# Kernel tuning notes

Measured on AMD Instinct MI355X. Metric: run time of the kernel, lower is better.

Reference implementation:

```python
import jax, jax.numpy as jnp
import numpy as np
import math

D_MODEL = 2048
NUM_HEADS = 16
D_HEAD = D_MODEL // NUM_HEADS
MAX_SEQ_LEN = 2048
THETA = 10000.0
B, T = 2, 2048


def setup_inputs() -> dict:
    key = jax.random.key(0)
    ks = jax.random.split(key, 5)
    s = 1.0 / math.sqrt(D_MODEL)
    return {
        "x": jax.random.normal(ks[0], (B, T, D_MODEL), dtype=jnp.float32),
        "token_positions": jnp.arange(T, dtype=jnp.int64 if jax.config.jax_enable_x64 else jnp.int32),
        "Wq": jax.random.normal(ks[1], (D_MODEL, D_MODEL), dtype=jnp.float32) * s,
        "Wk": jax.random.normal(ks[2], (D_MODEL, D_MODEL), dtype=jnp.float32) * s,
        "Wv": jax.random.normal(ks[3], (D_MODEL, D_MODEL), dtype=jnp.float32) * s,
        "Wproj": jax.random.normal(ks[4], (D_MODEL, D_MODEL), dtype=jnp.float32) * s,
    }


def _rope_tables(dtype):
    inv_freq = 1.0 / (THETA ** (jnp.arange(0, D_HEAD, 2, dtype=jnp.float32) / D_HEAD))
    angle = jnp.arange(MAX_SEQ_LEN, dtype=jnp.float32)[:, None] * inv_freq[None, :]  # [S, d/2]
    return jnp.cos(angle).astype(dtype), jnp.sin(angle).astype(dtype)


def _apply_rope(x, cos, sin):
    # x: [B, H, T, d_head]; cos/sin: [T, d_head/2] (broadcast over B,H)
    x1 = x[..., 0::2]
    x2 = x[..., 1::2]
    o1 = x1 * cos - x2 * sin
    o2 = x1 * sin + x2 * cos
    return jnp.stack([o1, o2], axis=-1).reshape(x.shape)


def reference(x, token_positions, Wq, Wk, Wv, Wproj):
    Bx, Tx, D = x.shape
    # Linear layers: weight [out, in], no bias
    q = (x @ Wq.T).reshape(Bx, Tx, NUM_HEADS, D_HEAD).transpose(0, 2, 1, 3)
    k = (x @ Wk.T).reshape(Bx, Tx, NUM_HEADS, D_HEAD).transpose(0, 2, 1, 3)
    v = (x @ Wv.T).reshape(Bx, Tx, NUM_HEADS, D_HEAD).transpose(0, 2, 1, 3)

    cos_t, sin_t = _rope_tables(x.dtype)
    cos = cos_t[token_positions]  # [T, d_head/2]
    sin = sin_t[token_positions]
    q = _apply_rope(q, cos, sin)
    k = _apply_rope(k, cos, sin)

    scale = 1.0 / math.sqrt(D_HEAD)
    scores = jnp.einsum("bhqd,bhkd->bhqk", q, k) * scale
    causal = jnp.tril(jnp.ones((Tx, Tx), dtype=bool))
    scores = jnp.where(causal, scores, -jnp.inf)
    attn = jax.nn.softmax(scores, axis=-1)
    o = jnp.einsum("bhqk,bhkd->bhqd", attn, v)  # [B, H, T, d_head]
    o = o.transpose(0, 2, 1, 3).reshape(Bx, Tx, D)
    return o @ Wproj.T
```

## Files before the change

### kernel.cpp

```cpp
#include <hip/hip_runtime.h>
#include <hip/hip_bf16.h>

#define DM    2048
#define NH    16
#define DHD   128
#define TSEQ  2048
#define NBB   2
#define NTOK  (NBB*TSEQ)

typedef __attribute__((ext_vector_type(8))) short bf16x8;
typedef __attribute__((ext_vector_type(4))) float f32x4;

typedef __attribute__((address_space(1))) const void GVoid;
typedef __attribute__((address_space(3))) void LVoid;
#define GLOAD16(SRC, DST) __builtin_amdgcn_global_load_lds((GVoid*)(SRC), (LVoid*)(DST), 16, 0, 0)

__device__ __forceinline__ unsigned short f2bf(float f) {
  union { float f; unsigned u; } v; v.f = f;
  unsigned r = v.u + 0x7fffu + ((v.u >> 16) & 1u);
  return (unsigned short)(r >> 16);
}
__device__ __forceinline__ float bf2f(unsigned short h) {
  union { unsigned u; float f; } v; v.u = ((unsigned)h) << 16;
  return v.f;
}

#define QSCALE (0.08838834764831845f * 1.4426950408889634f)

__global__ void cvt_kernel(const float* __restrict__ in, unsigned short* __restrict__ out, int n4) {
  int i = blockIdx.x * blockDim.x + threadIdx.x;
  int stride = gridDim.x * blockDim.x;
  for (; i < n4; i += stride) {
    float4 v = reinterpret_cast<const float4*>(in)[i];
    ushort4 o;
    o.x = f2bf(v.x); o.y = f2bf(v.y); o.z = f2bf(v.z); o.w = f2bf(v.w);
    reinterpret_cast<ushort4*>(out)[i] = o;
  }
}

__global__ void cvt4_kernel(const float* __restrict__ a, const float* __restrict__ b,
                           const float* __restrict__ c, const float* __restrict__ d,
                           unsigned short* __restrict__ out, int n4per) {
  const float* in = (blockIdx.y == 0) ? a : (blockIdx.y == 1) ? b : (blockIdx.y == 2) ? c : d;
  unsigned short* o = out + (size_t)blockIdx.y * (size_t)n4per * 4;
  int i = blockIdx.x * blockDim.x + threadIdx.x;
  int stride = gridDim.x * blockDim.x;
  for (; i < n4per; i += stride) {
    float4 v = reinterpret_cast<const float4*>(in)[i];
    ushort4 ov;
    ov.x = f2bf(v.x); ov.y = f2bf(v.y); ov.z = f2bf(v.z); ov.w = f2bf(v.w);
    reinterpret_cast<ushort4*>(o)[i] = ov;
  }
}

__global__ void rope_table_kernel(const int* __restrict__ pos, float* __restrict__ ctab, float* __restrict__ stab) {
  int idx = blockIdx.x * blockDim.x + threadIdx.x;
  if (idx >= TSEQ * 64) return;
  int i = idx & 63;
  int t = idx >> 6;
  float freq = expf(-(2.0f * i / 128.0f) * 9.210340371976184f);
  float ang = (float)pos[t] * freq;
  ctab[idx] = cosf(ang);
  stab[idx] = sinf(ang);
}

__global__ void vtrans_kernel(const unsigned short* __restrict__ Vb, unsigned short* __restrict__ VTt) {
  __shared__ unsigned short tile[32][33];
  int t0 = blockIdx.x * 32, d0 = blockIdx.y * 32, bh = blockIdx.z;
  int h = bh & (NH - 1), b = bh >> 4;
  int tx = threadIdx.x, ty = threadIdx.y;
  #pragma unroll
  for (int i = 0; i < 4; i++) {
    int tt = t0 + ty + i * 8;
    tile[ty + i * 8][tx] = Vb[(size_t)(b * TSEQ + tt) * DM + h * DHD + d0 + tx];
  }
  __syncthreads();
  #pragma unroll
  for (int i = 0; i < 4; i++) {
    int d = d0 + ty + i * 8;
    VTt[((size_t)bh * DHD + d) * TSEQ + t0 + tx] = tile[tx][ty + i * 8];
  }
}

#define GBM 128
#define GBN 256
#define GBK 32
#define LDSB ((GBM + GBN) * GBK)
template<int MODE>
__global__ __launch_bounds__(512, 4) void gemmk(
    const unsigned short* __restrict__ A,
    const unsigned short* __restrict__ Bt,
    void* __restrict__ Cp,
    unsigned short* __restrict__ QrO, unsigned short* __restrict__ KrO,
    const float* __restrict__ ct, const float* __restrict__ st,
    int K, int N, int NBN) {
  __shared__ unsigned short lds[3 * LDSB];
  const int t = threadIdx.x;
  const int lane = t & 63, w = t >> 6;
  const int wr = w >> 2, wc = w & 3;
  const int lr = lane & 15, lg = lane >> 4;
  const int nwg = gridDim.x;
  const int swz = (blockIdx.x & 7) * (nwg >> 3) + (blockIdx.x >> 3);
  const int m0 = (swz / NBN) * GBM;
  const int n0g = (swz % NBN) * GBN;
  const int NT = K / GBK;

  f32x4 acc[4][4] = {};

  auto stage = [&](int kt, int b) {
    unsigned short* dst = &lds[b * LDSB];
    const size_t k0 = (size_t)kt * GBK;
    {
      int row = t >> 2, slot = t & 3;
      int ss = slot ^ ((row >> 1) & 3);
      GLOAD16(A + (size_t)(m0 + row) * K + k0 + ss * 8, dst + (size_t)(w * 64) * 8);
    }
    unsigned short* dstB = dst + GBM * GBK;
    #pragma unroll
    for (int c = 0; c < 2; c++) {
      int ci = c * 512 + t;
      int row = ci >> 2, slot = ci & 3;
      int ss = slot ^ ((row >> 1) & 3);
      GLOAD16(Bt + (size_t)(n0g + row) * K + k0 + ss * 8, dstB + (size_t)(c * 512 + w * 64) * 8);
    }
  };

  const unsigned short* buf = nullptr;
  auto ldA = [&](int mi) -> bf16x8 {
    int r = wr * 64 + mi * 16 + lr;
    int cb = (lg * 16) ^ (((r >> 1) & 3) << 4);
    return *(const bf16x8*)((const char*)buf + r * 64 + cb);
  };
  auto ldB = [&](int ni) -> bf16x8 {
    int r = wc * 64 + ni * 16 + lr;
    int cb = (lg * 16) ^ (((r >> 1) & 3) << 4);
    return *(const bf16x8*)((const char*)(buf + GBM * GBK) + r * 64 + cb);
  };

  stage(0, 0);
  stage(1, 1);

  for (int kt = 0; kt < NT; kt++) {
    if (kt + 1 < NT) { asm volatile("s_waitcnt vmcnt(3)" ::: "memory"); }
    else             { asm volatile("s_waitcnt vmcnt(0)" ::: "memory"); }
    __builtin_amdgcn_s_barrier();
    buf = &lds[(kt % 3) * LDSB];

    bf16x8 bfr[4], afr[4];
    #pragma unroll
    for (int ni = 0; ni < 4; ni++) bfr[ni] = ldB(ni);
    #pragma unroll
    for (int mi = 0; mi < 4; mi++) afr[mi] = ldA(mi);
    if (kt + 2 < NT) stage(kt + 2, (kt + 2) % 3);
    asm volatile("s_waitcnt lgkmcnt(0)" ::: "memory");
    __builtin_amdgcn_sched_barrier(0);
    __builtin_amdgcn_s_setprio(1);
    #pragma unroll
    for (int mi = 0; mi < 4; mi++)
      #pragma unroll
      for (int ni = 0; ni < 4; ni++)
        acc[mi][ni] = __builtin_amdgcn_mfma_f32_16x16x32_bf16(afr[mi], bfr[ni], acc[mi][ni], 0, 0, 0);
    __builtin_amdgcn_s_setprio(0);
  }

  if (MODE == 0) {
    #pragma unroll
    for (int mi = 0; mi < 4; mi++)
      #pragma unroll
      for (int j = 0; j < 4; j++) {
        int row = m0 + wr * 64 + mi * 16 + lg * 4 + j;
        #pragma unroll
        for (int ni = 0; ni < 4; ni++) {
          int cg = n0g + wc * 64 + ni * 16 + lr;
          ((float*)Cp)[(size_t)row * N + cg] = acc[mi][ni][j];
        }
      }
  } else {
    const int sel = n0g >> 11;
    if (sel == 2) {
      #pragma unroll
      for (int mi = 0; mi < 4; mi++)
        #pragma unroll
        for (int j = 0; j < 4; j++) {
          int row = m0 + wr * 64 + mi * 16 + lg * 4 + j;
          #pragma unroll
          for (int ni = 0; ni < 4; ni++) {
            int c2 = (n0g + wc * 64 + ni * 16 + lr) & 2047;
            ((unsigned short*)Cp)[(size_t)row * DM + c2] = f2bf(acc[mi][ni][j]);
          }
        }
    } else {
      unsigned short* dst = sel ? KrO : QrO;
      const float qm = sel ? 1.0f : QSCALE;
      #pragma unroll
      for (int mi = 0; mi < 4; mi++)
        #pragma unroll
        for (int j = 0; j < 4; j++) {
          int row = m0 + wr * 64 + mi * 16 + lg * 4 + j;
          int bb = row >> 11, tt = row & (TSEQ - 1);
          #pragma unroll
          for (int ni = 0; ni < 4; ni++) {
            int c2 = (n0g + wc * 64 + ni * 16 + lr) & 2047;
            int d = c2 & 127, hh = c2 >> 7;
            float v = acc[mi][ni][j];
            float px = __shfl_xor(v, 1);
            float cc = ct[tt * 64 + (d >> 1)], ss = st[tt * 64 + (d >> 1)];
            float o = (d & 1) ? (px * ss + v * cc) : (v * cc - px * ss);
            dst[(((size_t)(bb * NH + hh)) * TSEQ + tt) * DHD + d] = f2bf(o * qm);
          }
        }
    }
  }
}

__global__ __launch_bounds__(512, 4) void attn_kernel(
    const unsigned short* __restrict__ Qr,
    const unsigned short* __restrict__ Kr,
    const unsigned short* __restrict__ VTt,
    unsigned short* __restrict__ Oa) {
  __shared__ unsigned short Ks[64 * 128];
  __shared__ unsigned short Vs[128 * 64];
  __shared__ unsigned short Ps[8 * 16 * 64];
  const int t = threadIdx.x;
  const int lane = t & 63, w = t >> 6;
  const int wv = w & 3, half = w >> 2;
  const int lr = lane & 15, lg = lane >> 4;
  const int p = blockIdx.x, bh = blockIdx.y;
  const int qA = p, qB = 31 - p;
  const int myq = half ? qA : qB;
  const int q0 = myq * 64;
  const int nt = myq + 1;
  const int ntB = qB + 1;
  const unsigned short* Qh = Qr + (size_t)bh * TSEQ * DHD;
  const unsigned short* Kh = Kr + (size_t)bh * TSEQ * DHD;
  const unsigned short* Vh = VTt + (size_t)bh * DHD * TSEQ;

  bf16x8 qf[4];
  #pragma unroll
  for (int ks = 0; ks < 4; ks++)
    qf[ks] = *(const bf16x8*)&Qh[((size_t)(q0 + wv * 16 + lr)) * DHD + ks * 32 + lg * 8];

  f32x4 oacc[8] = {};
  float ps[4] = {};
  unsigned short* Pw = &Ps[w * 16 * 64];

  for (int jt = 0; jt < ntB; jt++) {
    const int j0 = jt * 64;
    #pragma unroll
    for (int c = 0; c < 2; c++) {
      int ci = c * 512 + t;
      int row = ci >> 4, slot = ci & 15;
      GLOAD16(Kh + (size_t)(j0 + row) * DHD + (slot ^ (row & 7)) * 8,
              &Ks[(c * 512 + w * 64) * 8]);
    }
    #pragma unroll
    for (int c = 0; c < 2; c++) {
      int ci = c * 512 + t;
      int row = ci >> 3, slot = ci & 7;
      GLOAD16(Vh + (size_t)row * TSEQ + j0 + (slot ^ (row & 7)) * 8,
              &Vs[(c * 512 + w * 64) * 8]);
    }
    __syncthreads();
    if (jt < nt) {
      const bool diag = (jt == nt - 1);
      f32x4 sv[4] = {};
      #pragma unroll
      for (int n = 0; n < 4; n++) {
        #pragma unroll
        for (int ks = 0; ks < 4; ks++) {
          int row = n * 16 + lr;
          int byteoff = row * 256 + (((ks * 64 + lg * 16)) ^ ((row & 7) << 4));
          bf16x8 kf = *(const bf16x8*)((const char*)Ks + byteoff);
          sv[n] = __builtin_amdgcn_mfma_f32_16x16x32_bf16(qf[ks], kf, sv[n], 0, 0, 0);
        }
      }
      if (diag) {
        #pragma unroll
        for (int n = 0; n < 4; n++) {
          int kcol = j0 + n * 16 + lr;
          #pragma unroll
          for (int j = 0; j < 4; j++)
            if (kcol > q0 + wv * 16 + lg * 4 + j) sv[n][j] = -INFINITY;
        }
      }
      #pragma unroll
      for (int n = 0; n < 4; n++) {
        #pragma unroll
        for (int j = 0; j < 4; j++) {
          float pv = exp2f(sv[n][j]);
          ps[j] += pv;
          int prow = lg * 4 + j;
          int pcol = n * 16 + lr;
          int byteoff = (prow * 128 + pcol * 2) ^ ((prow & 7) << 4);
          *(unsigned short*)((char*)Pw + byteoff) = f2bf(pv);
        }
      }
      bf16x8 pa[2];
      #pragma unroll
      for (int kk = 0; kk < 2; kk++) {
        int byteoff = lr * 128 + (((kk * 64 + lg * 16)) ^ ((lr & 7) << 4));
        pa[kk] = *(const bf16x8*)((const char*)Pw + byteoff);
      }
      #pragma unroll
      for (int n2 = 0; n2 < 8; n2++) {
        #pragma unroll
        for (int kk = 0; kk < 2; kk++) {
          int row = n2 * 16 + lr;
          int byteoff = row * 128 + (((kk * 64 + lg * 16)) ^ ((row & 7) << 4));
          bf16x8 vf = *(const bf16x8*)((const char*)Vs + byteoff);
          oacc[n2] = __builtin_amdgcn_mfma_f32_16x16x32_bf16(pa[kk], vf, oacc[n2], 0, 0, 0);
        }
      }
    }
    __syncthreads();
  }

  #pragma unroll
  for (int m = 1; m < 16; m <<= 1)
    #pragma unroll
    for (int j = 0; j < 4; j++) ps[j] += __shfl_xor(ps[j], m);
  const int h = bh & (NH - 1), b = bh >> 4;
  #pragma unroll
  for (int j = 0; j < 4; j++) {
    float inv = 1.0f / ps[j];
    int tt = q0 + wv * 16 + lg * 4 + j;
    size_t base = ((size_t)(b * TSEQ + tt)) * DM + h * DHD;
    #pragma unroll
    for (int n2 = 0; n2 < 8; n2++)
      Oa[base + n2 * 16 + lr] = f2bf(oacc[n2][j] * inv);
  }
}

extern "C" void kernel_launch(void* const* d_in, const int* in_sizes, int n_in,
                              void* d_out, int out_size, void* d_ws, size_t ws_size,
                              hipStream_t stream) {
  const float* x  = (const float*)d_in[0];
  const int*   pos = (const int*)d_in[1];
  const float* Wq = (const float*)d_in[2];
  const float* Wk = (const float*)d_in[3];
  const float* Wv = (const float*)d_in[4];
  const float* Wp = (const float*)d_in[5];
  float* out = (float*)d_out;

  char* wsp = (char*)d_ws;
  auto alloc = [&](size_t bytes) { char* p = wsp; wsp += (bytes + 255) & ~(size_t)255; return p; };
  unsigned short* xb  = (unsigned short*)alloc((size_t)NTOK * DM * 2);
  unsigned short* wqb = (unsigned short*)alloc((size_t)DM * DM * 2);
  unsigned short* wkb = (unsigned short*)alloc((size_t)DM * DM * 2);
  unsigned short* wvb = (unsigned short*)alloc((size_t)DM * DM * 2);
  unsigned short* wpb = (unsigned short*)alloc((size_t)DM * DM * 2);
  unsigned short* Qb  = (unsigned short*)alloc((size_t)NTOK * DM * 2);
  unsigned short* Kb  = (unsigned short*)alloc((size_t)NTOK * DM * 2);
  unsigned short* Vb  = (unsigned short*)alloc((size_t)NTOK * DM * 2);
  unsigned short* VTt = (unsigned short*)alloc((size_t)NTOK * DM * 2);
  float* ctab = (float*)alloc((size_t)TSEQ * 64 * 4);
  float* stab = (float*)alloc((size_t)TSEQ * 64 * 4);
  unsigned short* Oa = xb;
  (void)wkb; (void)wvb;

  int n4x = NTOK * DM / 4, n4w = DM * DM / 4;
  cvt_kernel<<<2048, 256, 0, stream>>>(x, xb, n4x);
  cvt4_kernel<<<dim3(256, 4), 256, 0, stream>>>(Wq, Wk, Wv, Wp, wqb, n4w);
  rope_table_kernel<<<(TSEQ * 64) / 256, 256, 0, stream>>>(pos, ctab, stab);

  gemmk<1><<<(NTOK / GBM) * (3 * DM / GBN), 512, 0, stream>>>(
      xb, wqb, Vb, Qb, Kb, ctab, stab, DM, DM, 3 * DM / GBN);

  vtrans_kernel<<<dim3(TSEQ / 32, DHD / 32, NBB * NH), dim3(32, 8), 0, stream>>>(Vb, VTt);

  attn_kernel<<<dim3(16, NBB * NH), 512, 0, stream>>>(Qb, Kb, VTt, Oa);

  gemmk<0><<<(NTOK / GBM) * (DM / GBN), 512, 0, stream>>>(
      Oa, wpb, out, nullptr, nullptr, nullptr, nullptr, DM, DM, DM / GBN);
}
```

Baseline: 260.3 us.

## Split attention KV range across half-blocks and add 256x128 output GEMM

Attention now launches one block per (query tile, head) in descending-work order instead of pairing two query tiles per block. The two halves of the block each process half of the causal KV tiles using double LDS buffers, and their partial outputs and row sums are merged through LDS at the end. This is meant to improve load balance and parallelism. The output projection switches to a new 256x128-tile GEMM with a triple-buffered global-to-LDS pipeline and priority-raised MFMA phases. The costs are more blocks, an extra LDS reduction step, and higher LDS use.

```diff
diff --git a/kernel.cpp b/kernel.cpp
--- a/kernel.cpp
+++ b/kernel.cpp
@@ -213,24 +213,150 @@
   }
 }
 
+#define G2M 256
+#define G2N 128
+#define G2K 64
+__global__ __launch_bounds__(512, 2) void gemm256(
+    const unsigned short* __restrict__ A,
+    const unsigned short* __restrict__ Bt,
+    float* __restrict__ Cp, int K, int N, int NBN) {
+  __shared__ unsigned short lds[3 * (G2M + G2N) * G2K];
+  const int t = threadIdx.x;
+  const int lane = t & 63, w = t >> 6;
+  const int wr = w >> 2, wc = w & 3;
+  const int lr = lane & 15, lg = lane >> 4;
+  const int nwg = gridDim.x;
+  const int swz = (blockIdx.x & 7) * (nwg >> 3) + (blockIdx.x >> 3);
+  const int m0 = (swz / NBN) * G2M;
+  const int n0g = (swz % NBN) * G2N;
+  const int NT = K / G2K;
+
+  f32x4 acc[8][2] = {};
+
+  auto stageA = [&](int kt, int b) {
+    unsigned short* dst = &lds[b * (G2M + G2N) * G2K];
+    const size_t k0 = (size_t)kt * G2K;
+    #pragma unroll
+    for (int c = 0; c < 4; c++) {
+      int i = c * 512 + t;
+      int row = i >> 3, slot = i & 7;
+      int sslot = slot ^ (row & 7);
+      GLOAD16(A + (size_t)(m0 + row) * K + k0 + sslot * 8,
+              dst + (size_t)(c * 512 + w * 64) * 8);
+    }
+  };
+  auto stageB = [&](int kt, int b) {
+    unsigned short* dst = &lds[b * (G2M + G2N) * G2K + G2M * G2K];
+    const size_t k0 = (size_t)kt * G2K;
+    #pragma unroll
+    for (int c = 0; c < 2; c++) {
+      int i = c * 512 + t;
+      int row = i >> 3, slot = i & 7;
+      int sslot = slot ^ (row & 7);
+      GLOAD16(Bt + (size_t)(n0g + row) * K + k0 + sslot * 8,
+              dst + (size_t)(c * 512 + w * 64) * 8);
+    }
+  };
+
+  const unsigned short* bufA = nullptr;
+  const unsigned short* bufB = nullptr;
+  auto ldA = [&](int mi, int ks) -> bf16x8 {
+    int r = wr * 128 + mi * 16 + lr;
+    int cb = (ks * 64 + lg * 16) ^ ((r & 7) << 4);
+    return *(const bf16x8*)((const char*)bufA + r * 128 + cb);
+  };
+  auto ldB = [&](int ni, int ks) -> bf16x8 {
+    int r = wc * 32 + ni * 16 + lr;
+    int cb = (ks * 64 + lg * 16) ^ ((r & 7) << 4);
+    return *(const bf16x8*)((const char*)bufB + r * 128 + cb);
+  };
+
+  stageA(0, 0); stageB(0, 0);
+  stageA(1, 1); stageB(1, 1);
+
+  for (int kt = 0; kt < NT; kt++) {
+    if (kt + 1 < NT) { asm volatile("s_waitcnt vmcnt(6)" ::: "memory"); }
+    else             { asm volatile("s_waitcnt vmcnt(0)" ::: "memory"); }
+    __builtin_amdgcn_s_barrier();
+    const int b = kt % 3;
+    bufA = &lds[b * (G2M + G2N) * G2K];
+    bufB = bufA + G2M * G2K;
+    const int kt2 = kt + 2, b2 = kt2 % 3;
+
+    bf16x8 bfr[2][2], afr[4][2];
+    #pragma unroll
+    for (int ni = 0; ni < 2; ni++)
+      #pragma unroll
+      for (int ks = 0; ks < 2; ks++) bfr[ni][ks] = ldB(ni, ks);
+    #pragma unroll
+    for (int mi = 0; mi < 4; mi++)
+      #pragma unroll
+      for (int ks = 0; ks < 2; ks++) afr[mi][ks] = ldA(mi, ks);
+    if (kt2 < NT) stageA(kt2, b2);
+    asm volatile("s_waitcnt lgkmcnt(0)" ::: "memory");
+    __builtin_amdgcn_sched_barrier(0);
+    __builtin_amdgcn_s_setprio(1);
+    #pragma unroll
+    for (int mi = 0; mi < 4; mi++)
+      #pragma unroll
+      for (int ni = 0; ni < 2; ni++)
+        #pragma unroll
+        for (int ks = 0; ks < 2; ks++)
+          acc[mi][ni] = __builtin_amdgcn_mfma_f32_16x16x32_bf16(afr[mi][ks], bfr[ni][ks], acc[mi][ni], 0, 0, 0);
+    __builtin_amdgcn_s_setprio(0);
+    __builtin_amdgcn_s_barrier();
+
+    bf16x8 afr2[4][2];
+    #pragma unroll
+    for (int mi = 0; mi < 4; mi++)
+      #pragma unroll
+      for (int ks = 0; ks < 2; ks++) afr2[mi][ks] = ldA(mi + 4, ks);
+    if (kt2 < NT) stageB(kt2, b2);
+    asm volatile("s_waitcnt lgkmcnt(0)" ::: "memory");
+    __builtin_amdgcn_sched_barrier(0);
+    __builtin_amdgcn_s_setprio(1);
+    #pragma unroll
+    for (int mi = 0; mi < 4; mi++)
+      #pragma unroll
+      for (int ni = 0; ni < 2; ni++)
+        #pragma unroll
+        for (int ks = 0; ks < 2; ks++)
+          acc[mi + 4][ni] = __builtin_amdgcn_mfma_f32_16x16x32_bf16(afr2[mi][ks], bfr[ni][ks], acc[mi + 4][ni], 0, 0, 0);
+    __builtin_amdgcn_s_setprio(0);
+  }
+
+  #pragma unroll
+  for (int mi = 0; mi < 8; mi++)
+    #pragma unroll
+    for (int j = 0; j < 4; j++) {
+      int row = m0 + wr * 128 + mi * 16 + lg * 4 + j;
+      #pragma unroll
+      for (int ni = 0; ni < 2; ni++) {
+        int cg = n0g + wc * 32 + ni * 16 + lr;
+        Cp[(size_t)row * N + cg] = acc[mi][ni][j];
+      }
+    }
+}
+
 __global__ __launch_bounds__(512, 4) void attn_kernel(
     const unsigned short* __restrict__ Qr,
     const unsigned short* __restrict__ Kr,
     const unsigned short* __restrict__ VTt,
     unsigned short* __restrict__ Oa) {
-  __shared__ unsigned short Ks[64 * 128];
-  __shared__ unsigned short Vs[128 * 64];
+  __shared__ unsigned short Ks[2][64 * 128];
+  __shared__ unsigned short Vs[2][128 * 64];
   __shared__ unsigned short Ps[8 * 16 * 64];
   const int t = threadIdx.x;
   const int lane = t & 63, w = t >> 6;
   const int wv = w & 3, half = w >> 2;
+  const int th = t & 255;
   const int lr = lane & 15, lg = lane >> 4;
-  const int p = blockIdx.x, bh = blockIdx.y;
-  const int qA = p, qB = 31 - p;
-  const int myq = half ? qA : qB;
-  const int q0 = myq * 64;
-  const int nt = myq + 1;
-  const int ntB = qB + 1;
+  const int bid = blockIdx.x;
+  const int qi = 31 - (bid >> 5);
+  const int bh = bid & 31;
+  const int q0 = qi * 64;
+  const int ntot = qi + 1;
+  const int n0 = (ntot + 1) >> 1;
   const unsigned short* Qh = Qr + (size_t)bh * TSEQ * DHD;
   const unsigned short* Kh = Kr + (size_t)bh * TSEQ * DHD;
   const unsigned short* Vh = VTt + (size_t)bh * DHD * TSEQ;
@@ -244,25 +370,30 @@
   float ps[4] = {};
   unsigned short* Pw = &Ps[w * 16 * 64];
 
-  for (int jt = 0; jt < ntB; jt++) {
-    const int j0 = jt * 64;
-    #pragma unroll
-    for (int c = 0; c < 2; c++) {
-      int ci = c * 512 + t;
-      int row = ci >> 4, slot = ci & 15;
-      GLOAD16(Kh + (size_t)(j0 + row) * DHD + (slot ^ (row & 7)) * 8,
-              &Ks[(c * 512 + w * 64) * 8]);
-    }
-    #pragma unroll
-    for (int c = 0; c < 2; c++) {
-      int ci = c * 512 + t;
-      int row = ci >> 3, slot = ci & 7;
-      GLOAD16(Vh + (size_t)row * TSEQ + j0 + (slot ^ (row & 7)) * 8,
-              &Vs[(c * 512 + w * 64) * 8]);
+  for (int jt = 0; jt < n0; jt++) {
+    const int j = half ? (n0 + jt) : jt;
+    const bool act = j < ntot;
+    if (act) {
+      const int j0 = j * 64;
+      #pragma unroll
+      for (int c = 0; c < 4; c++) {
+        int ci = c * 256 + th;
+        int row = ci >> 4, slot = ci & 15;
+        GLOAD16(Kh + (size_t)(j0 + row) * DHD + (slot ^ (row & 7)) * 8,
+                &Ks[half][(c * 4 + wv) * 512]);
+      }
+      #pragma unroll
+      for (int c = 0; c < 4; c++) {
+        int ci = c * 256 + th;
+        int row = ci >> 3, slot = ci & 7;
+        GLOAD16(Vh + (size_t)row * TSEQ + j0 + (slot ^ (row & 7)) * 8,
+                &Vs[half][(c * 4 + wv) * 512]);
+      }
     }
     __syncthreads();
-    if (jt < nt) {
-      const bool diag = (jt == nt - 1);
+    if (act) {
+      const int j0 = j * 64;
+      const bool diag = (j == qi);
       f32x4 sv[4] = {};
       #pragma unroll
       for (int n = 0; n < 4; n++) {
@@ -270,7 +401,7 @@
         for (int ks = 0; ks < 4; ks++) {
           int row = n * 16 + lr;
           int byteoff = row * 256 + (((ks * 64 + lg * 16)) ^ ((row & 7) << 4));
-          bf16x8 kf = *(const bf16x8*)((const char*)Ks + byteoff);
+          bf16x8 kf = *(const bf16x8*)((const char*)&Ks[half][0] + byteoff);
           sv[n] = __builtin_amdgcn_mfma_f32_16x16x32_bf16(qf[ks], kf, sv[n], 0, 0, 0);
         }
       }
@@ -279,17 +410,17 @@
         for (int n = 0; n < 4; n++) {
           int kcol = j0 + n * 16 + lr;
           #pragma unroll
-          for (int j = 0; j < 4; j++)
-            if (kcol > q0 + wv * 16 + lg * 4 + j) sv[n][j] = -INFINITY;
+          for (int j2 = 0; j2 < 4; j2++)
+            if (kcol > q0 + wv * 16 + lg * 4 + j2) sv[n][j2] = -INFINITY;
         }
       }
       #pragma unroll
       for (int n = 0; n < 4; n++) {
         #pragma unroll
-        for (int j = 0; j < 4; j++) {
-          float pv = exp2f(sv[n][j]);
-          ps[j] += pv;
-          int prow = lg * 4 + j;
+        for (int j2 = 0; j2 < 4; j2++) {
+          float pv = exp2f(sv[n][j2]);
+          ps[j2] += pv;
+          int prow = lg * 4 + j2;
           int pcol = n * 16 + lr;
           int byteoff = (prow * 128 + pcol * 2) ^ ((prow & 7) << 4);
           *(unsigned short*)((char*)Pw + byteoff) = f2bf(pv);
@@ -307,7 +438,7 @@
         for (int kk = 0; kk < 2; kk++) {
           int row = n2 * 16 + lr;
           int byteoff = row * 128 + (((kk * 64 + lg * 16)) ^ ((row & 7) << 4));
-          bf16x8 vf = *(const bf16x8*)((const char*)Vs + byteoff);
+          bf16x8 vf = *(const bf16x8*)((const char*)&Vs[half][0] + byteoff);
           oacc[n2] = __builtin_amdgcn_mfma_f32_16x16x32_bf16(pa[kk], vf, oacc[n2], 0, 0, 0);
         }
       }
@@ -315,19 +446,41 @@
     __syncthreads();
   }
 
-  #pragma unroll
-  for (int m = 1; m < 16; m <<= 1)
-    #pragma unroll
-    for (int j = 0; j < 4; j++) ps[j] += __shfl_xor(ps[j], m);
-  const int h = bh & (NH - 1), b = bh >> 4;
-  #pragma unroll
-  for (int j = 0; j < 4; j++) {
-    float inv = 1.0f / ps[j];
-    int tt = q0 + wv * 16 + lg * 4 + j;
-    size_t base = ((size_t)(b * TSEQ + tt)) * DM + h * DHD;
+  float* M  = (float*)&Ks[0][0];
+  float* P2 = (float*)&Vs[0][0];
+  if (half == 1) {
     #pragma unroll
     for (int n2 = 0; n2 < 8; n2++)
-      Oa[base + n2 * 16 + lr] = f2bf(oacc[n2][j] * inv);
+      #pragma unroll
+      for (int j = 0; j < 4; j++)
+        M[((wv * 16 + lg * 4 + j) * 8 + n2) * 16 + lr] = oacc[n2][j];
+    #pragma unroll
+    for (int j = 0; j < 4; j++)
+      P2[(wv * 16 + lg * 4 + j) * 16 + lr] = ps[j];
+  }
+  __syncthreads();
+  if (half == 0) {
+    #pragma unroll
+    for (int n2 = 0; n2 < 8; n2++)
+      #pragma unroll
+      for (int j = 0; j < 4; j++)
+        oacc[n2][j] += M[((wv * 16 + lg * 4 + j) * 8 + n2) * 16 + lr];
+    #pragma unroll
+    for (int j = 0; j < 4; j++) ps[j] += P2[(wv * 16 + lg * 4 + j) * 16 + lr];
+    #pragma unroll
+    for (int m = 1; m < 16; m <<= 1)
+      #pragma unroll
+      for (int j = 0; j < 4; j++) ps[j] += __shfl_xor(ps[j], m);
+    const int h = bh & (NH - 1), b = bh >> 4;
+    #pragma unroll
+    for (int j = 0; j < 4; j++) {
+      float inv = 1.0f / ps[j];
+      int tt = q0 + wv * 16 + lg * 4 + j;
+      size_t base = ((size_t)(b * TSEQ + tt)) * DM + h * DHD;
+      #pragma unroll
+      for (int n2 = 0; n2 < 8; n2++)
+        Oa[base + n2 * 16 + lr] = f2bf(oacc[n2][j] * inv);
+    }
   }
 }
 
@@ -368,8 +521,7 @@
 
   vtrans_kernel<<<dim3(TSEQ / 32, DHD / 32, NBB * NH), dim3(32, 8), 0, stream>>>(Vb, VTt);
 
-  attn_kernel<<<dim3(16, NBB * NH), 512, 0, stream>>>(Qb, Kb, VTt, Oa);
-
-  gemmk<0><<<(NTOK / GBM) * (DM / GBN), 512, 0, stream>>>(
-      Oa, wpb, out, nullptr, nullptr, nullptr, nullptr, DM, DM, DM / GBN);
-}
+  attn_kernel<<<1024, 512, 0, stream>>>(Qb, Kb, VTt, Oa);
+
+  gemm256<<<(NTOK / G2M) * (DM / G2N), 512, 0, stream>>>(Oa, wpb, out, DM, DM, DM / G2N);
+}
```

Measured after the change: 256.0 us. About the same (-1.6%).
